# Optimization experiments

Measured on AMD Instinct MI355X. Metric: run time of the kernel, lower is better.

The kernel has to match this reference:

```python
import jax, jax.numpy as jnp
import numpy as np

N_NODES = 100000
N_EDGES = 500000
N_RELS = 200
N_BASE = 50
INIT_D = 100
FEAT_D = 128
N_CLS = 50
N_LAYERS = 2
BN_EPS = 1e-5


def setup_inputs() -> dict:
    key = jax.random.key(0)
    ks = jax.random.split(key, 16)
    inp = {
        'edge_src': jax.random.randint(ks[0], (N_LAYERS, N_EDGES), 0, N_NODES),
        'edge_dst': jax.random.randint(ks[1], (N_LAYERS, N_EDGES), 0, N_NODES),
        'edge_type': jax.random.randint(ks[2], (N_LAYERS, N_EDGES), 0, N_RELS),
        'emb_h': jax.random.normal(ks[3], (N_NODES, INIT_D), jnp.float32),
        'emb_e': jax.random.normal(ks[4], (N_BASE, INIT_D), jnp.float32),
        'rel_wt': jax.random.normal(ks[5], (N_RELS, N_BASE), jnp.float32) * 0.1,
        'W_h_init': jax.random.normal(ks[6], (INIT_D, FEAT_D), jnp.float32) * (1.0 / np.sqrt(INIT_D)),
        'W_e_init': jax.random.normal(ks[7], (INIT_D, FEAT_D), jnp.float32) * (1.0 / np.sqrt(INIT_D)),
        'aggre_W': jax.random.normal(ks[8], (FEAT_D, FEAT_D), jnp.float32) * (1.0 / np.sqrt(FEAT_D)),
        'aggre_b': jnp.zeros((FEAT_D,), jnp.float32),
        'bn_gamma': jnp.ones((FEAT_D,), jnp.float32),
        'bn_beta': jnp.zeros((FEAT_D,), jnp.float32),
        'fc0_w': jax.random.normal(ks[9], (FEAT_D, FEAT_D // 2), jnp.float32) * (1.0 / np.sqrt(FEAT_D)),
        'fc0_b': jnp.zeros((FEAT_D // 2,), jnp.float32),
        'fc1_w': jax.random.normal(ks[10], (FEAT_D // 2, FEAT_D // 4), jnp.float32) * (1.0 / np.sqrt(FEAT_D // 2)),
        'fc1_b': jnp.zeros((FEAT_D // 4,), jnp.float32),
        'fc2_w': jax.random.normal(ks[11], (FEAT_D // 4, N_CLS), jnp.float32) * (1.0 / np.sqrt(FEAT_D // 4)),
        'fc2_b': jnp.zeros((N_CLS,), jnp.float32),
    }
    return inp


def _segment_mean(msg, dst, num_segments):
    # mean reduction of per-edge messages into dst nodes (DGL reduce_mean)
    sums = jax.ops.segment_sum(msg, dst, num_segments=num_segments)
    cnt = jax.ops.segment_sum(jnp.ones((msg.shape[0], 1), msg.dtype), dst,
                              num_segments=num_segments)
    return sums / jnp.maximum(cnt, 1.0)


def _forward(emb_h, emb_e, rel_wt, W_h_init, W_e_init, aggre_W, aggre_b,
             bn_gamma, bn_beta, fc0_w, fc0_b, fc1_w, fc1_b, fc2_w, fc2_b,
             edge_src, edge_dst, edge_type):
    node_embed = None
    for i in range(N_LAYERS):
        src, dst, etype = edge_src[i], edge_dst[i], edge_type[i]
        if i == 0:
            # embedding gather + init projection: [E, init_d] @ [init_d, feat]
            src_emb = emb_h[src] @ W_h_init
        else:
            src_emb = node_embed[src]
        # relation-weight mixing: rel_wt[etype] @ emb_e, then init projection
        edges_embed = (rel_wt[etype] @ emb_e) @ W_e_init  # [E, feat]
        # message = relu(linear(src)) composed with relation embedding
        msg = jax.nn.relu(src_emb @ aggre_W + aggre_b) + edges_embed
        node_embed = _segment_mean(msg, dst, N_NODES)
    # batchnorm over node dim (training batch stats)
    mu = jnp.mean(node_embed, axis=0)
    var = jnp.var(node_embed, axis=0)
    h = (node_embed - mu) * jax.lax.rsqrt(var + BN_EPS) * bn_gamma + bn_beta
    h = jax.nn.relu(h)
    # MLP classifier: 128 -> 64 -> 32 -> num_classes
    h = jax.nn.relu(h @ fc0_w + fc0_b)
    h = jax.nn.relu(h @ fc1_w + fc1_b)
    logits = h @ fc2_w + fc2_b
    return logits


def reference(edge_src, edge_dst, edge_type, emb_h, emb_e, rel_wt, W_h_init,
              W_e_init, aggre_W, aggre_b, bn_gamma, bn_beta, fc0_w, fc0_b,
              fc1_w, fc1_b, fc2_w, fc2_b):
    return _forward(emb_h, emb_e, rel_wt, W_h_init, W_e_init, aggre_W,
                    aggre_b, bn_gamma, bn_beta, fc0_w, fc0_b, fc1_w, fc1_b,
                    fc2_w, fc2_b, edge_src, edge_dst, edge_type)
```

## Files before the change

### kernel.cpp

```cpp
#include <hip/hip_runtime.h>
#include <cstdint>
#include <cstddef>

#define N_NODES 100000
#define N_EDGES 500000
#define N_RELS  200
#define N_BASE  50
#define INIT_D  100
#define FEAT_D  128
#define N_CLS   50
#define BN_EPS  1e-5f

#define SCAN_BLK 1024
#define NB_SCAN  ((N_NODES + SCAN_BLK - 1) / SCAN_BLK)

typedef unsigned int uint;
typedef unsigned short ushort;

__device__ inline uint packbf2(float a, float b) {
  uint ua = __float_as_uint(a); ua = (ua + 0x7fffu + ((ua >> 16) & 1u)) >> 16;
  uint ub = __float_as_uint(b); ub = (ub + 0x7fffu + ((ub >> 16) & 1u)) >> 16;
  return ua | (ub << 16);
}
__device__ inline float bf_lo(uint u) { return __uint_as_float(u << 16); }
__device__ inline float bf_hi(uint u) { return __uint_as_float(u & 0xffff0000u); }

__global__ __launch_bounds__(128)
void rel_kernel(const float* __restrict__ rel_wt, const float* __restrict__ emb_e,
                const float* __restrict__ W_e, float* __restrict__ REL) {
  int r = blockIdx.x;
  int t = threadIdx.x;
  __shared__ float T[INIT_D];
  if (t < INIT_D) {
    float a = 0.f;
    for (int b = 0; b < N_BASE; ++b)
      a += rel_wt[r * N_BASE + b] * emb_e[b * INIT_D + t];
    T[t] = a;
  }
  __syncthreads();
  float a = 0.f;
  for (int k = 0; k < INIT_D; ++k)
    a += T[k] * W_e[k * FEAT_D + t];
  REL[r * FEAT_D + t] = a;
}

__global__ __launch_bounds__(128)
void wcomb_kernel(const float* __restrict__ W_h, const float* __restrict__ aggre_W,
                  float* __restrict__ WC) {
  int i = blockIdx.x;
  int j = threadIdx.x;
  __shared__ float row[FEAT_D];
  row[j] = W_h[i * FEAT_D + j];
  __syncthreads();
  float a = 0.f;
  for (int f = 0; f < FEAT_D; ++f)
    a += row[f] * aggre_W[f * FEAT_D + j];
  WC[i * FEAT_D + j] = a;
}

__global__ __launch_bounds__(256)
void h0_kernel(const float* __restrict__ emb_h, const float* __restrict__ WC,
               const float* __restrict__ bias, ushort* __restrict__ H, int nNodes) {
  __shared__ float WT[FEAT_D * INIT_D];
  __shared__ float bs[FEAT_D];
  int t = threadIdx.x;
  for (int i = t; i < FEAT_D * INIT_D; i += 256) {
    int k = i >> 7, j = i & 127;
    WT[j * INIT_D + k] = WC[i];
  }
  if (t < FEAT_D) bs[t] = bias[t];
  __syncthreads();
  for (int n = blockIdx.x * 256 + t; n < nNodes; n += gridDim.x * 256) {
    float x[INIT_D];
    const float4* xp = (const float4*)(emb_h + (size_t)n * INIT_D);
#pragma unroll
    for (int q = 0; q < 25; ++q) {
      float4 v = xp[q];
      x[4 * q + 0] = v.x; x[4 * q + 1] = v.y; x[4 * q + 2] = v.z; x[4 * q + 3] = v.w;
    }
    uint2* orow = (uint2*)(H + (size_t)n * FEAT_D);
    for (int j4 = 0; j4 < 32; ++j4) {
      float4 a;
      a.x = bs[4 * j4 + 0]; a.y = bs[4 * j4 + 1];
      a.z = bs[4 * j4 + 2]; a.w = bs[4 * j4 + 3];
      const float4* w0 = (const float4*)&WT[(4 * j4 + 0) * INIT_D];
      const float4* w1 = (const float4*)&WT[(4 * j4 + 1) * INIT_D];
      const float4* w2 = (const float4*)&WT[(4 * j4 + 2) * INIT_D];
      const float4* w3 = (const float4*)&WT[(4 * j4 + 3) * INIT_D];
#pragma unroll
      for (int q = 0; q < 25; ++q) {
        float4 v0 = w0[q], v1 = w1[q], v2 = w2[q], v3 = w3[q];
        a.x = fmaf(x[4*q+0], v0.x, a.x); a.x = fmaf(x[4*q+1], v0.y, a.x);
        a.x = fmaf(x[4*q+2], v0.z, a.x); a.x = fmaf(x[4*q+3], v0.w, a.x);
        a.y = fmaf(x[4*q+0], v1.x, a.y); a.y = fmaf(x[4*q+1], v1.y, a.y);
        a.y = fmaf(x[4*q+2], v1.z, a.y); a.y = fmaf(x[4*q+3], v1.w, a.y);
        a.z = fmaf(x[4*q+0], v2.x, a.z); a.z = fmaf(x[4*q+1], v2.y, a.z);
        a.z = fmaf(x[4*q+2], v2.z, a.z); a.z = fmaf(x[4*q+3], v2.w, a.z);
        a.w = fmaf(x[4*q+0], v3.x, a.w); a.w = fmaf(x[4*q+1], v3.y, a.w);
        a.w = fmaf(x[4*q+2], v3.z, a.w); a.w = fmaf(x[4*q+3], v3.w, a.w);
      }
      a.x = fmaxf(a.x, 0.f); a.y = fmaxf(a.y, 0.f);
      a.z = fmaxf(a.z, 0.f); a.w = fmaxf(a.w, 0.f);
      uint2 pk; pk.x = packbf2(a.x, a.y); pk.y = packbf2(a.z, a.w);
      orow[j4] = pk;
    }
  }
}

__global__ __launch_bounds__(256)
void hist_kernel(const int* __restrict__ dst, int* __restrict__ deg, int nEdges) {
  for (int e = blockIdx.x * 256 + threadIdx.x; e < nEdges; e += gridDim.x * 256)
    atomicAdd(&deg[dst[e]], 1);
}

__global__ __launch_bounds__(256)
void scanA_kernel(const int* __restrict__ deg, int* __restrict__ bsum, int n) {
  __shared__ int red[256];
  int t = threadIdx.x;
  int base = blockIdx.x * SCAN_BLK + t * 4;
  int s = 0;
#pragma unroll
  for (int q = 0; q < 4; ++q) {
    int i = base + q;
    s += (i < n) ? deg[i] : 0;
  }
  red[t] = s;
  __syncthreads();
  for (int off = 128; off > 0; off >>= 1) {
    if (t < off) red[t] += red[t + off];
    __syncthreads();
  }
  if (t == 0) bsum[blockIdx.x] = red[0];
}

__global__ void scanB_kernel(int* __restrict__ bsum, int nb, int* __restrict__ off) {
  int run = 0;
  for (int i = 0; i < nb; ++i) {
    int v = bsum[i];
    bsum[i] = run;
    run += v;
  }
  off[N_NODES] = run;
}

__global__ __launch_bounds__(256)
void scanC_kernel(const int* __restrict__ deg, const int* __restrict__ bsum,
                  int* __restrict__ off, int* __restrict__ cur, int n) {
  __shared__ int lds[256];
  int t = threadIdx.x;
  int base = blockIdx.x * SCAN_BLK + t * 4;
  int d[4];
  int s = 0;
#pragma unroll
  for (int q = 0; q < 4; ++q) {
    int i = base + q;
    d[q] = (i < n) ? deg[i] : 0;
    s += d[q];
  }
  lds[t] = s;
  __syncthreads();
  for (int o = 1; o < 256; o <<= 1) {
    int v = (t >= o) ? lds[t - o] : 0;
    __syncthreads();
    lds[t] += v;
    __syncthreads();
  }
  int excl = lds[t] - s + bsum[blockIdx.x];
#pragma unroll
  for (int q = 0; q < 4; ++q) {
    int i = base + q;
    if (i < n) {
      off[i] = excl;
      cur[i] = excl;
    }
    excl += d[q];
  }
}

__global__ __launch_bounds__(256)
void fill_kernel(const int* __restrict__ src, const int* __restrict__ dst,
                 const int* __restrict__ et, int* __restrict__ cur,
                 int* __restrict__ epk, int nEdges) {
  for (int e = blockIdx.x * 256 + threadIdx.x; e < nEdges; e += gridDim.x * 256) {
    int d = dst[e];
    int pos = atomicAdd(&cur[d], 1);
    epk[pos] = src[e] | (et[e] << 17);
  }
}

__global__ __launch_bounds__(256)
void gather_mean_kernel(const int* __restrict__ off, const int* __restrict__ epk,
                        const ushort* __restrict__ H, const float* __restrict__ REL,
                        float* __restrict__ MEAN, int doBN, float* __restrict__ acc,
                        int nNodes) {
  const uint2* H2 = (const uint2*)H;
  const float4* R4 = (const float4*)REL;
  float4* M4 = (float4*)MEAN;
  int t = threadIdx.x;
  int j = t & 31;
  int slot = t >> 5;
  float4 s1 = {0.f, 0.f, 0.f, 0.f}, s2 = {0.f, 0.f, 0.f, 0.f};
  for (int n = blockIdx.x * 8 + slot; n < nNodes; n += gridDim.x * 8) {
    int beg = off[n], end = off[n + 1];
    float4 a = {0.f, 0.f, 0.f, 0.f};
    int p = beg;
#pragma unroll 1
    for (; p + 4 <= end; p += 4) {
      int u0 = epk[p + 0];
      int u1 = epk[p + 1];
      int u2 = epk[p + 2];
      int u3 = epk[p + 3];
      uint2 h0 = H2[(size_t)(u0 & 0x1FFFF) * 32 + j];
      uint2 h1 = H2[(size_t)(u1 & 0x1FFFF) * 32 + j];
      uint2 h2 = H2[(size_t)(u2 & 0x1FFFF) * 32 + j];
      uint2 h3 = H2[(size_t)(u3 & 0x1FFFF) * 32 + j];
      float4 r0 = R4[(u0 >> 17) * 32 + j];
      float4 r1 = R4[(u1 >> 17) * 32 + j];
      float4 r2 = R4[(u2 >> 17) * 32 + j];
      float4 r3 = R4[(u3 >> 17) * 32 + j];
      a.x += (bf_lo(h0.x) + r0.x) + (bf_lo(h1.x) + r1.x) +
             (bf_lo(h2.x) + r2.x) + (bf_lo(h3.x) + r3.x);
      a.y += (bf_hi(h0.x) + r0.y) + (bf_hi(h1.x) + r1.y) +
             (bf_hi(h2.x) + r2.y) + (bf_hi(h3.x) + r3.y);
      a.z += (bf_lo(h0.y) + r0.z) + (bf_lo(h1.y) + r1.z) +
             (bf_lo(h2.y) + r2.z) + (bf_lo(h3.y) + r3.z);
      a.w += (bf_hi(h0.y) + r0.w) + (bf_hi(h1.y) + r1.w) +
             (bf_hi(h2.y) + r2.w) + (bf_hi(h3.y) + r3.w);
    }
#pragma unroll 1
    for (; p < end; ++p) {
      int u = epk[p];
      uint2 hv = H2[(size_t)(u & 0x1FFFF) * 32 + j];
      float4 rv = R4[(u >> 17) * 32 + j];
      a.x += bf_lo(hv.x) + rv.x; a.y += bf_hi(hv.x) + rv.y;
      a.z += bf_lo(hv.y) + rv.z; a.w += bf_hi(hv.y) + rv.w;
    }
    float rd = (end > beg) ? 1.f / (float)(end - beg) : 0.f;
    a.x *= rd; a.y *= rd; a.z *= rd; a.w *= rd;
    M4[(size_t)n * 32 + j] = a;
    if (doBN) {
      s1.x += a.x; s1.y += a.y; s1.z += a.z; s1.w += a.w;
      s2.x += a.x * a.x; s2.y += a.y * a.y;
      s2.z += a.z * a.z; s2.w += a.w * a.w;
    }
  }
  if (doBN) {
    __shared__ float4 r1[8][32], r2[8][32];
    r1[slot][j] = s1;
    r2[slot][j] = s2;
    __syncthreads();
    if (slot == 0) {
      float4 a1 = r1[0][j], a2 = r2[0][j];
#pragma unroll
      for (int k = 1; k < 8; ++k) {
        float4 b1 = r1[k][j], b2 = r2[k][j];
        a1.x += b1.x; a1.y += b1.y; a1.z += b1.z; a1.w += b1.w;
        a2.x += b2.x; a2.y += b2.y; a2.z += b2.z; a2.w += b2.w;
      }
      atomicAdd(&acc[4 * j + 0], a1.x);
      atomicAdd(&acc[4 * j + 1], a1.y);
      atomicAdd(&acc[4 * j + 2], a1.z);
      atomicAdd(&acc[4 * j + 3], a1.w);
      atomicAdd(&acc[FEAT_D + 4 * j + 0], a2.x);
      atomicAdd(&acc[FEAT_D + 4 * j + 1], a2.y);
      atomicAdd(&acc[FEAT_D + 4 * j + 2], a2.z);
      atomicAdd(&acc[FEAT_D + 4 * j + 3], a2.w);
    }
  }
}

__global__ __launch_bounds__(256)
void h1_kernel(const float* __restrict__ mean, const float* __restrict__ W,
               const float* __restrict__ bias, ushort* __restrict__ H, int nNodes) {
  __shared__ float WT[FEAT_D * FEAT_D];
  __shared__ float bs[FEAT_D];
  int t = threadIdx.x;
  for (int i = t; i < FEAT_D * FEAT_D; i += 256) {
    int k = i >> 7, j = i & 127;
    WT[j * FEAT_D + k] = W[i];
  }
  if (t < FEAT_D) bs[t] = bias[t];
  __syncthreads();
  for (int n = blockIdx.x * 256 + t; n < nNodes; n += gridDim.x * 256) {
    float x[FEAT_D];
    const float4* xp = (const float4*)(mean + (size_t)n * FEAT_D);
#pragma unroll
    for (int q = 0; q < 32; ++q) {
      float4 v = xp[q];
      x[4 * q + 0] = v.x; x[4 * q + 1] = v.y;
      x[4 * q + 2] = v.z; x[4 * q + 3] = v.w;
    }
    uint2* orow = (uint2*)(H + (size_t)n * FEAT_D);
    for (int j4 = 0; j4 < 32; ++j4) {
      float4 a;
      a.x = bs[4 * j4 + 0]; a.y = bs[4 * j4 + 1];
      a.z = bs[4 * j4 + 2]; a.w = bs[4 * j4 + 3];
      const float4* w0 = (const float4*)&WT[(4 * j4 + 0) * FEAT_D];
      const float4* w1 = (const float4*)&WT[(4 * j4 + 1) * FEAT_D];
      const float4* w2 = (const float4*)&WT[(4 * j4 + 2) * FEAT_D];
      const float4* w3 = (const float4*)&WT[(4 * j4 + 3) * FEAT_D];
#pragma unroll
      for (int q = 0; q < 32; ++q) {
        float4 v0 = w0[q], v1 = w1[q], v2 = w2[q], v3 = w3[q];
        a.x = fmaf(x[4*q+0], v0.x, a.x); a.x = fmaf(x[4*q+1], v0.y, a.x);
        a.x = fmaf(x[4*q+2], v0.z, a.x); a.x = fmaf(x[4*q+3], v0.w, a.x);
        a.y = fmaf(x[4*q+0], v1.x, a.y); a.y = fmaf(x[4*q+1], v1.y, a.y);
        a.y = fmaf(x[4*q+2], v1.z, a.y); a.y = fmaf(x[4*q+3], v1.w, a.y);
        a.z = fmaf(x[4*q+0], v2.x, a.z); a.z = fmaf(x[4*q+1], v2.y, a.z);
        a.z = fmaf(x[4*q+2], v2.z, a.z); a.z = fmaf(x[4*q+3], v2.w, a.z);
        a.w = fmaf(x[4*q+0], v3.x, a.w); a.w = fmaf(x[4*q+1], v3.y, a.w);
        a.w = fmaf(x[4*q+2], v3.z, a.w); a.w = fmaf(x[4*q+3], v3.w, a.w);
      }
      a.x = fmaxf(a.x, 0.f); a.y = fmaxf(a.y, 0.f);
      a.z = fmaxf(a.z, 0.f); a.w = fmaxf(a.w, 0.f);
      uint2 pk; pk.x = packbf2(a.x, a.y); pk.y = packbf2(a.z, a.w);
      orow[j4] = pk;
    }
  }
}

__global__ __launch_bounds__(256)
void final_kernel(const float* __restrict__ mean, const float* __restrict__ acc,
                  const float* __restrict__ gamma, const float* __restrict__ beta,
                  const float* __restrict__ fc0w, const float* __restrict__ fc0b,
                  const float* __restrict__ fc1w, const float* __restrict__ fc1b,
                  const float* __restrict__ fc2w, const float* __restrict__ fc2b,
                  float* __restrict__ out, int nNodes) {
  __shared__ float W0T[64 * FEAT_D];
  __shared__ float W1L[64 * 32];
  __shared__ float W2T[N_CLS * 32];
  __shared__ float sc[FEAT_D], sh[FEAT_D];
  __shared__ float b0[64], b1[32], b2[N_CLS];
  int t = threadIdx.x;
  for (int i = t; i < 64 * FEAT_D; i += 256) {
    int k = i >> 6, j = i & 63;
    W0T[j * FEAT_D + k] = fc0w[i];
  }
  for (int i = t; i < 64 * 32; i += 256) W1L[i] = fc1w[i];
  for (int i = t; i < 32 * N_CLS; i += 256) {
    int jj = i / N_CLS, c = i % N_CLS;
    W2T[c * 32 + jj] = fc2w[i];
  }
  if (t < FEAT_D) {
    float m = acc[t] * (1.f / (float)N_NODES);
    float v = acc[FEAT_D + t] * (1.f / (float)N_NODES) - m * m;
    float r = rsqrtf(v + BN_EPS);
    float g = gamma[t];
    sc[t] = r * g;
    sh[t] = beta[t] - m * r * g;
  }
  if (t < 64) b0[t] = fc0b[t];
  if (t < 32) b1[t] = fc1b[t];
  if (t < N_CLS) b2[t] = fc2b[t];
  __syncthreads();
  for (int n = blockIdx.x * 256 + t; n < nNodes; n += gridDim.x * 256) {
    float x[FEAT_D];
    const float4* xp = (const float4*)(mean + (size_t)n * FEAT_D);
#pragma unroll
    for (int q = 0; q < 32; ++q) {
      float4 v = xp[q];
      x[4*q+0] = fmaxf(fmaf(v.x, sc[4*q+0], sh[4*q+0]), 0.f);
      x[4*q+1] = fmaxf(fmaf(v.y, sc[4*q+1], sh[4*q+1]), 0.f);
      x[4*q+2] = fmaxf(fmaf(v.z, sc[4*q+2], sh[4*q+2]), 0.f);
      x[4*q+3] = fmaxf(fmaf(v.w, sc[4*q+3], sh[4*q+3]), 0.f);
    }
    float acc2[32];
#pragma unroll
    for (int jj = 0; jj < 32; ++jj) acc2[jj] = b1[jj];
    for (int j = 0; j < 64; ++j) {
      float a = b0[j];
      const float4* w = (const float4*)&W0T[j * FEAT_D];
#pragma unroll
      for (int q = 0; q < 32; ++q) {
        float4 v = w[q];
        a = fmaf(x[4*q+0], v.x, a); a = fmaf(x[4*q+1], v.y, a);
        a = fmaf(x[4*q+2], v.z, a); a = fmaf(x[4*q+3], v.w, a);
      }
      float h = fmaxf(a, 0.f);
      const float4* w1 = (const float4*)&W1L[j * 32];
#pragma unroll
      for (int q = 0; q < 8; ++q) {
        float4 v = w1[q];
        acc2[4*q+0] = fmaf(h, v.x, acc2[4*q+0]);
        acc2[4*q+1] = fmaf(h, v.y, acc2[4*q+1]);
        acc2[4*q+2] = fmaf(h, v.z, acc2[4*q+2]);
        acc2[4*q+3] = fmaf(h, v.w, acc2[4*q+3]);
      }
    }
    float h2[32];
#pragma unroll
    for (int jj = 0; jj < 32; ++jj) h2[jj] = fmaxf(acc2[jj], 0.f);
    float* orow = out + (size_t)n * N_CLS;
    for (int cc = 0; cc < N_CLS; ++cc) {
      float a = b2[cc];
      const float4* w = (const float4*)&W2T[cc * 32];
#pragma unroll
      for (int q = 0; q < 8; ++q) {
        float4 v = w[q];
        a = fmaf(h2[4*q+0], v.x, a); a = fmaf(h2[4*q+1], v.y, a);
        a = fmaf(h2[4*q+2], v.z, a); a = fmaf(h2[4*q+3], v.w, a);
      }
      orow[cc] = a;
    }
  }
}

extern "C" void kernel_launch(void* const* d_in, const int* in_sizes, int n_in,
                              void* d_out, int out_size, void* d_ws, size_t ws_size,
                              hipStream_t stream) {
  const int* edge_src = (const int*)d_in[0];
  const int* edge_dst = (const int*)d_in[1];
  const int* edge_type = (const int*)d_in[2];
  const float* emb_h = (const float*)d_in[3];
  const float* emb_e = (const float*)d_in[4];
  const float* rel_wt = (const float*)d_in[5];
  const float* W_h_init = (const float*)d_in[6];
  const float* W_e_init = (const float*)d_in[7];
  const float* aggre_W = (const float*)d_in[8];
  const float* aggre_b = (const float*)d_in[9];
  const float* bn_gamma = (const float*)d_in[10];
  const float* bn_beta = (const float*)d_in[11];
  const float* fc0_w = (const float*)d_in[12];
  const float* fc0_b = (const float*)d_in[13];
  const float* fc1_w = (const float*)d_in[14];
  const float* fc1_b = (const float*)d_in[15];
  const float* fc2_w = (const float*)d_in[16];
  const float* fc2_b = (const float*)d_in[17];
  float* out = (float*)d_out;

  char* ws = (char*)d_ws;
  float*  REL  = (float*)(ws);
  float*  WC   = (float*)(ws + 102400);
  ushort* H    = (ushort*)(ws + 153600);
  float*  MEAN = (float*)(ws + 25753600);
  float*  ACC  = (float*)(ws + 76953600);

  char* ob = (char*)d_out;
  int* EPK  = (int*)(ob);
  int* DEG  = (int*)(ob + 2000000);
  int* OFF  = (int*)(ob + 2400000);
  int* CUR  = (int*)(ob + 2800004);
  int* BSUM = (int*)(ob + 3200008);

  const int NODE_BLOCKS = (N_NODES + 255) / 256;
  const int GATHER_BLOCKS = 2048;

  hipMemsetAsync(ACC, 0, 1024, stream);

  rel_kernel<<<N_RELS, 128, 0, stream>>>(rel_wt, emb_e, W_e_init, REL);
  wcomb_kernel<<<INIT_D, 128, 0, stream>>>(W_h_init, aggre_W, WC);
  h0_kernel<<<NODE_BLOCKS, 256, 0, stream>>>(emb_h, WC, aggre_b, H, N_NODES);

  hipMemsetAsync(DEG, 0, 400000, stream);
  hist_kernel<<<1024, 256, 0, stream>>>(edge_dst, DEG, N_EDGES);
  scanA_kernel<<<NB_SCAN, 256, 0, stream>>>(DEG, BSUM, N_NODES);
  scanB_kernel<<<1, 1, 0, stream>>>(BSUM, NB_SCAN, OFF);
  scanC_kernel<<<NB_SCAN, 256, 0, stream>>>(DEG, BSUM, OFF, CUR, N_NODES);
  fill_kernel<<<1024, 256, 0, stream>>>(edge_src, edge_dst, edge_type, CUR, EPK,
                                        N_EDGES);
  gather_mean_kernel<<<GATHER_BLOCKS, 256, 0, stream>>>(OFF, EPK, H, REL, MEAN, 0,
                                                        ACC, N_NODES);

  h1_kernel<<<NODE_BLOCKS, 256, 0, stream>>>(MEAN, aggre_W, aggre_b, H, N_NODES);

  hipMemsetAsync(DEG, 0, 400000, stream);
  hist_kernel<<<1024, 256, 0, stream>>>(edge_dst + N_EDGES, DEG, N_EDGES);
  scanA_kernel<<<NB_SCAN, 256, 0, stream>>>(DEG, BSUM, N_NODES);
  scanB_kernel<<<1, 1, 0, stream>>>(BSUM, NB_SCAN, OFF);
  scanC_kernel<<<NB_SCAN, 256, 0, stream>>>(DEG, BSUM, OFF, CUR, N_NODES);
  fill_kernel<<<1024, 256, 0, stream>>>(edge_src + N_EDGES, edge_dst + N_EDGES,
                                        edge_type + N_EDGES, CUR, EPK, N_EDGES);
  gather_mean_kernel<<<GATHER_BLOCKS, 256, 0, stream>>>(OFF, EPK, H, REL, MEAN, 1,
                                                        ACC, N_NODES);

  final_kernel<<<NODE_BLOCKS, 256, 0, stream>>>(MEAN, ACC, bn_gamma, bn_beta,
                                                fc0_w, fc0_b, fc1_w, fc1_b,
                                                fc2_w, fc2_b, out, N_NODES);
}
```

Before: 760.6 us.

## Fuse setup kernels, fold memsets into node kernels, single-block scan

Merges the relation and weight-combination kernels into one launch. The DEG and ACC zeroing moves into h0_kernel and h1_kernel, which replaces the memsets. The three-kernel scan (block sums, serial prefix, apply) becomes one 1024-thread single-block scan over int4 loads. The aim is to cut launch count and the serial scanB step. The risks are that the single-block scan runs on one CU and is serial, and that zeroing DEG in h1 relies on stream ordering after the first gather has finished reading it.

```diff
diff --git a/kernel.cpp b/kernel.cpp
--- a/kernel.cpp
+++ b/kernel.cpp
@@ -11,9 +11,6 @@
 #define N_CLS   50
 #define BN_EPS  1e-5f
 
-#define SCAN_BLK 1024
-#define NB_SCAN  ((N_NODES + SCAN_BLK - 1) / SCAN_BLK)
-
 typedef unsigned int uint;
 typedef unsigned short ushort;
 
@@ -26,44 +23,48 @@
 __device__ inline float bf_hi(uint u) { return __uint_as_float(u & 0xffff0000u); }
 
 __global__ __launch_bounds__(128)
-void rel_kernel(const float* __restrict__ rel_wt, const float* __restrict__ emb_e,
-                const float* __restrict__ W_e, float* __restrict__ REL) {
-  int r = blockIdx.x;
-  int t = threadIdx.x;
-  __shared__ float T[INIT_D];
-  if (t < INIT_D) {
+void relwc_kernel(const float* __restrict__ rel_wt, const float* __restrict__ emb_e,
+                  const float* __restrict__ W_e, float* __restrict__ REL,
+                  const float* __restrict__ W_h, const float* __restrict__ aggre_W,
+                  float* __restrict__ WC) {
+  __shared__ float T[FEAT_D];
+  int t = threadIdx.x;
+  if (blockIdx.x < N_RELS) {
+    int r = blockIdx.x;
+    if (t < INIT_D) {
+      float a = 0.f;
+      for (int b = 0; b < N_BASE; ++b)
+        a += rel_wt[r * N_BASE + b] * emb_e[b * INIT_D + t];
+      T[t] = a;
+    }
+    __syncthreads();
     float a = 0.f;
-    for (int b = 0; b < N_BASE; ++b)
-      a += rel_wt[r * N_BASE + b] * emb_e[b * INIT_D + t];
-    T[t] = a;
-  }
-  __syncthreads();
-  float a = 0.f;
-  for (int k = 0; k < INIT_D; ++k)
-    a += T[k] * W_e[k * FEAT_D + t];
-  REL[r * FEAT_D + t] = a;
-}
-
-__global__ __launch_bounds__(128)
-void wcomb_kernel(const float* __restrict__ W_h, const float* __restrict__ aggre_W,
-                  float* __restrict__ WC) {
-  int i = blockIdx.x;
-  int j = threadIdx.x;
-  __shared__ float row[FEAT_D];
-  row[j] = W_h[i * FEAT_D + j];
-  __syncthreads();
-  float a = 0.f;
-  for (int f = 0; f < FEAT_D; ++f)
-    a += row[f] * aggre_W[f * FEAT_D + j];
-  WC[i * FEAT_D + j] = a;
+    for (int k = 0; k < INIT_D; ++k)
+      a += T[k] * W_e[k * FEAT_D + t];
+    REL[r * FEAT_D + t] = a;
+  } else {
+    int i = blockIdx.x - N_RELS;
+    T[t] = W_h[i * FEAT_D + t];
+    __syncthreads();
+    float a = 0.f;
+    for (int f = 0; f < FEAT_D; ++f)
+      a += T[f] * aggre_W[f * FEAT_D + t];
+    WC[i * FEAT_D + t] = a;
+  }
 }
 
 __global__ __launch_bounds__(256)
 void h0_kernel(const float* __restrict__ emb_h, const float* __restrict__ WC,
-               const float* __restrict__ bias, ushort* __restrict__ H, int nNodes) {
+               const float* __restrict__ bias, ushort* __restrict__ H,
+               int* __restrict__ deg, float* __restrict__ acc, int nNodes) {
   __shared__ float WT[FEAT_D * INIT_D];
   __shared__ float bs[FEAT_D];
   int t = threadIdx.x;
+  {
+    int g = blockIdx.x * 256 + t;
+    if (g < N_NODES) deg[g] = 0;
+    if (g < 2 * FEAT_D) acc[g] = 0.f;
+  }
   for (int i = t; i < FEAT_D * INIT_D; i += 256) {
     int k = i >> 7, j = i & 127;
     WT[j * INIT_D + k] = WC[i];
@@ -113,68 +114,48 @@
     atomicAdd(&deg[dst[e]], 1);
 }
 
-__global__ __launch_bounds__(256)
-void scanA_kernel(const int* __restrict__ deg, int* __restrict__ bsum, int n) {
-  __shared__ int red[256];
-  int t = threadIdx.x;
-  int base = blockIdx.x * SCAN_BLK + t * 4;
+__global__ __launch_bounds__(1024)
+void scan_fused_kernel(const int* __restrict__ deg, int* __restrict__ off,
+                       int* __restrict__ cur) {
+  __shared__ int psum[1024];
+  const int4* deg4 = (const int4*)deg;
+  int t = threadIdx.x;
+  const int N4 = N_NODES / 4;
   int s = 0;
-#pragma unroll
-  for (int q = 0; q < 4; ++q) {
-    int i = base + q;
-    s += (i < n) ? deg[i] : 0;
-  }
-  red[t] = s;
+#pragma unroll 1
+  for (int q = 0; q < 25; ++q) {
+    int i4 = t * 25 + q;
+    if (i4 < N4) {
+      int4 v = deg4[i4];
+      s += v.x + v.y + v.z + v.w;
+    }
+  }
+  psum[t] = s;
   __syncthreads();
-  for (int off = 128; off > 0; off >>= 1) {
-    if (t < off) red[t] += red[t + off];
+#pragma unroll 1
+  for (int o = 1; o < 1024; o <<= 1) {
+    int v = (t >= o) ? psum[t - o] : 0;
     __syncthreads();
-  }
-  if (t == 0) bsum[blockIdx.x] = red[0];
-}
-
-__global__ void scanB_kernel(int* __restrict__ bsum, int nb, int* __restrict__ off) {
-  int run = 0;
-  for (int i = 0; i < nb; ++i) {
-    int v = bsum[i];
-    bsum[i] = run;
-    run += v;
-  }
-  off[N_NODES] = run;
-}
-
-__global__ __launch_bounds__(256)
-void scanC_kernel(const int* __restrict__ deg, const int* __restrict__ bsum,
-                  int* __restrict__ off, int* __restrict__ cur, int n) {
-  __shared__ int lds[256];
-  int t = threadIdx.x;
-  int base = blockIdx.x * SCAN_BLK + t * 4;
-  int d[4];
-  int s = 0;
-#pragma unroll
-  for (int q = 0; q < 4; ++q) {
-    int i = base + q;
-    d[q] = (i < n) ? deg[i] : 0;
-    s += d[q];
-  }
-  lds[t] = s;
-  __syncthreads();
-  for (int o = 1; o < 256; o <<= 1) {
-    int v = (t >= o) ? lds[t - o] : 0;
+    psum[t] += v;
     __syncthreads();
-    lds[t] += v;
-    __syncthreads();
-  }
-  int excl = lds[t] - s + bsum[blockIdx.x];
-#pragma unroll
-  for (int q = 0; q < 4; ++q) {
-    int i = base + q;
-    if (i < n) {
-      off[i] = excl;
-      cur[i] = excl;
-    }
-    excl += d[q];
-  }
+  }
+  int run = psum[t] - s;
+#pragma unroll 1
+  for (int q = 0; q < 25; ++q) {
+    int i4 = t * 25 + q;
+    if (i4 < N4) {
+      int4 v = deg4[i4];
+      int4 o4;
+      o4.x = run;
+      o4.y = run + v.x;
+      o4.z = run + v.x + v.y;
+      o4.w = run + v.x + v.y + v.z;
+      ((int4*)off)[i4] = o4;
+      ((int4*)cur)[i4] = o4;
+      run += v.x + v.y + v.z + v.w;
+    }
+  }
+  if (t == 1023) off[N_NODES] = psum[1023];
 }
 
 __global__ __launch_bounds__(256)
@@ -271,10 +252,15 @@
 
 __global__ __launch_bounds__(256)
 void h1_kernel(const float* __restrict__ mean, const float* __restrict__ W,
-               const float* __restrict__ bias, ushort* __restrict__ H, int nNodes) {
+               const float* __restrict__ bias, ushort* __restrict__ H,
+               int* __restrict__ deg, int nNodes) {
   __shared__ float WT[FEAT_D * FEAT_D];
   __shared__ float bs[FEAT_D];
   int t = threadIdx.x;
+  {
+    int g = blockIdx.x * 256 + t;
+    if (g < N_NODES) deg[g] = 0;
+  }
   for (int i = t; i < FEAT_D * FEAT_D; i += 256) {
     int k = i >> 7, j = i & 127;
     WT[j * FEAT_D + k] = W[i];
@@ -440,34 +426,27 @@
   int* DEG  = (int*)(ob + 2000000);
   int* OFF  = (int*)(ob + 2400000);
   int* CUR  = (int*)(ob + 2800004);
-  int* BSUM = (int*)(ob + 3200008);
 
   const int NODE_BLOCKS = (N_NODES + 255) / 256;
   const int GATHER_BLOCKS = 2048;
 
-  hipMemsetAsync(ACC, 0, 1024, stream);
-
-  rel_kernel<<<N_RELS, 128, 0, stream>>>(rel_wt, emb_e, W_e_init, REL);
-  wcomb_kernel<<<INIT_D, 128, 0, stream>>>(W_h_init, aggre_W, WC);
-  h0_kernel<<<NODE_BLOCKS, 256, 0, stream>>>(emb_h, WC, aggre_b, H, N_NODES);
-
-  hipMemsetAsync(DEG, 0, 400000, stream);
+  relwc_kernel<<<N_RELS + INIT_D, 128, 0, stream>>>(rel_wt, emb_e, W_e_init, REL,
+                                                    W_h_init, aggre_W, WC);
+  h0_kernel<<<NODE_BLOCKS, 256, 0, stream>>>(emb_h, WC, aggre_b, H, DEG, ACC,
+                                             N_NODES);
+
   hist_kernel<<<1024, 256, 0, stream>>>(edge_dst, DEG, N_EDGES);
-  scanA_kernel<<<NB_SCAN, 256, 0, stream>>>(DEG, BSUM, N_NODES);
-  scanB_kernel<<<1, 1, 0, stream>>>(BSUM, NB_SCAN, OFF);
-  scanC_kernel<<<NB_SCAN, 256, 0, stream>>>(DEG, BSUM, OFF, CUR, N_NODES);
+  scan_fused_kernel<<<1, 1024, 0, stream>>>(DEG, OFF, CUR);
   fill_kernel<<<1024, 256, 0, stream>>>(edge_src, edge_dst, edge_type, CUR, EPK,
                                         N_EDGES);
   gather_mean_kernel<<<GATHER_BLOCKS, 256, 0, stream>>>(OFF, EPK, H, REL, MEAN, 0,
                                                         ACC, N_NODES);
 
-  h1_kernel<<<NODE_BLOCKS, 256, 0, stream>>>(MEAN, aggre_W, aggre_b, H, N_NODES);
-
-  hipMemsetAsync(DEG, 0, 400000, stream);
+  h1_kernel<<<NODE_BLOCKS, 256, 0, stream>>>(MEAN, aggre_W, aggre_b, H, DEG,
+                                             N_NODES);
+
   hist_kernel<<<1024, 256, 0, stream>>>(edge_dst + N_EDGES, DEG, N_EDGES);
-  scanA_kernel<<<NB_SCAN, 256, 0, stream>>>(DEG, BSUM, N_NODES);
-  scanB_kernel<<<1, 1, 0, stream>>>(BSUM, NB_SCAN, OFF);
-  scanC_kernel<<<NB_SCAN, 256, 0, stream>>>(DEG, BSUM, OFF, CUR, N_NODES);
+  scan_fused_kernel<<<1, 1024, 0, stream>>>(DEG, OFF, CUR);
   fill_kernel<<<1024, 256, 0, stream>>>(edge_src + N_EDGES, edge_dst + N_EDGES,
                                         edge_type + N_EDGES, CUR, EPK, N_EDGES);
   gather_mean_kernel<<<GATHER_BLOCKS, 256, 0, stream>>>(OFF, EPK, H, REL, MEAN, 1,
```

Result: slower. 870.3 us (+14.4%).
